# Kernel optimization log

Hardware: AMD Instinct MI355X
Metric: run time of the kernel (lower is better)

Reference implementation:

```python
import jax, jax.numpy as jnp
import numpy as np

B, N, C = 16, 4096, 1024
K = 64
TEMPERATURE = 1.0


def setup_inputs() -> dict:
    key = jax.random.key(0)
    kx, kw = jax.random.split(key)
    x = jax.random.normal(kx, (B, N, C), dtype=jnp.float32)
    # nn.Linear(dim, dim): W is (out, in), b is (out,)
    W = jax.random.normal(kw, (C, C), dtype=jnp.float32) * (1.0 / np.sqrt(C))
    b = jnp.zeros((C,), dtype=jnp.float32)
    return {"x": x, "W": W, "b": b}


def reference(x, W, b):
    Bv, Nv, Cv = x.shape
    # proj = x @ W.T + b ; scores = proj.mean(-1)  -> fold mean into a single matvec:
    # mean(x W^T + b) = x @ (mean of W rows) + mean(b), but keep faithful/explicit form.
    proj = jnp.einsum('bnc,dc->bnd', x, W) + b          # (B, N, C)
    scores = jnp.mean(proj, axis=-1)                    # (B, N)
    k = min(K, Nv)
    _, topk_idx = jax.lax.top_k(scores, k)              # (B, k)
    mask = jnp.zeros_like(scores).at[jnp.arange(Bv)[:, None], topk_idx].set(1.0)
    attn = jax.nn.softmax(scores / TEMPERATURE, axis=-1) * mask  # (B, N)
    out = jnp.einsum('bn,bnc->bc', attn, x)             # (B, C)
    return out, mask
```

## Files before the change

kernel.cpp:

```cpp
#include <hip/hip_runtime.h>
#include <cstdint>

#define B_ 16
#define N_ 4096
#define C_ 1024
#define K_ 64

typedef float vf4 __attribute__((ext_vector_type(4)));

#define WS_WBAR   0
#define WS_BBAR   1024
#define WS_SCORES 2048
#define WS_TIDX   (WS_SCORES + B_*N_)
#define WS_TATT   (WS_TIDX + B_*K_)
#define WS_PART   (WS_TATT + B_*K_)

__global__ __launch_bounds__(256) void wsum1_kernel(const float* __restrict__ W,
                                                    const float* __restrict__ b,
                                                    float* __restrict__ ws) {
    int j = blockIdx.x, t = threadIdx.x;
    if (j == 64) {
        float4 bv = ((const float4*)b)[t];
        float sb = bv.x + bv.y + bv.z + bv.w;
        for (int off = 32; off; off >>= 1) sb += __shfl_xor(sb, off);
        __shared__ float red[4];
        if ((t & 63) == 0) red[t >> 6] = sb;
        __syncthreads();
        if (t == 0) ws[WS_BBAR] = (red[0] + red[1] + red[2] + red[3]) * (1.0f / C_);
        return;
    }
    const float4* W4 = (const float4*)W;
    float4 s = {0.f, 0.f, 0.f, 0.f};
#pragma unroll
    for (int d = 0; d < 16; ++d) {
        float4 w = W4[(j * 16 + d) * 256 + t];
        s.x += w.x; s.y += w.y; s.z += w.z; s.w += w.w;
    }
    ((float4*)(ws + WS_PART))[j * 256 + t] = s;
}

__global__ __launch_bounds__(256) void wsum2_kernel(float* __restrict__ ws) {
    int col = blockIdx.x * 256 + threadIdx.x;
    float s = 0.f;
#pragma unroll 8
    for (int j = 0; j < 64; ++j) s += ws[WS_PART + j * 1024 + col];
    ws[WS_WBAR + col] = s * (1.0f / C_);
}

__global__ __launch_bounds__(512) void scores_kernel(const float* __restrict__ x,
                                                     float* ws) {
    __shared__ float lw[C_];
    int t = threadIdx.x;
    float bbar = ws[WS_BBAR];
    if (t < 256) ((float4*)lw)[t] = ((const float4*)(ws + WS_WBAR))[t];
    __syncthreads();
    int wave = t >> 6, lane = t & 63;
    int row = blockIdx.x * 8 + wave;
    const vf4* x4 = (const vf4*)x;
    const float4* lw4 = (const float4*)lw;
    float acc = 0.f;
#pragma unroll
    for (int q = 0; q < 4; ++q) {
        vf4 xv = __builtin_nontemporal_load(x4 + (size_t)row * 256 + q * 64 + lane);
        float4 wv = lw4[q * 64 + lane];
        acc += xv.x * wv.x + xv.y * wv.y + xv.z * wv.z + xv.w * wv.w;
    }
    for (int off = 32; off; off >>= 1) acc += __shfl_xor(acc, off);
    if (lane == 0) ws[WS_SCORES + row] = acc + bbar;
}

__device__ __forceinline__ unsigned su_(float f) {
    unsigned u = __float_as_uint(f);
    return (u & 0x80000000u) ? ~u : (u | 0x80000000u);
}
__device__ __forceinline__ float isu_(unsigned u) {
    unsigned v = (u & 0x80000000u) ? (u ^ 0x80000000u) : ~u;
    return __uint_as_float(v);
}

__global__ __launch_bounds__(256) void topk_kernel(float* ws,
                                                   float* __restrict__ mask_out) {
    __shared__ unsigned hist[4096];
    __shared__ unsigned long long cand[4096];
    __shared__ float redf[4];
    __shared__ unsigned scnt;
    __shared__ int sbin;
    int b = blockIdx.x, t = threadIdx.x;
    int wid = t >> 6, lane = t & 63;
    const float* srow = ws + WS_SCORES + b * N_;

    float v[16];
#pragma unroll
    for (int e = 0; e < 16; ++e) v[e] = srow[e * 256 + t];

#pragma unroll
    for (int e = 0; e < 16; ++e) hist[e * 256 + t] = 0;
    if (t == 0) scnt = 0;

    float m = v[0];
#pragma unroll
    for (int e = 1; e < 16; ++e) m = fmaxf(m, v[e]);
    for (int off = 32; off; off >>= 1) m = fmaxf(m, __shfl_xor(m, off));
    if (lane == 0) redf[wid] = m;
    __syncthreads();
    m = fmaxf(fmaxf(redf[0], redf[1]), fmaxf(redf[2], redf[3]));

    float dsum = 0.f;
#pragma unroll
    for (int e = 0; e < 16; ++e) dsum += expf(v[e] - m);
    for (int off = 32; off; off >>= 1) dsum += __shfl_xor(dsum, off);

#pragma unroll
    for (int e = 0; e < 16; ++e) atomicAdd(&hist[su_(v[e]) >> 20], 1u);

    __syncthreads();
    if (lane == 0) redf[wid] = dsum;
    __syncthreads();
    float denom = redf[0] + redf[1] + redf[2] + redf[3];

    if (wid == 0) {
        int base = lane * 64;
        unsigned s = 0;
        for (int j = 0; j < 64; ++j) s += hist[base + j];
        unsigned suf = s;
        for (int off = 1; off < 64; off <<= 1) {
            unsigned o = __shfl_down(suf, off);
            if (lane + off < 64) suf += o;
        }
        unsigned above = suf - s;
        if (above < (unsigned)K_ && above + s >= (unsigned)K_) {
            unsigned run = above;
            for (int j = 63; j >= 0; --j) {
                unsigned c = hist[base + j];
                if (run < (unsigned)K_ && run + c >= (unsigned)K_) sbin = base + j;
                run += c;
            }
        }
    }
    __syncthreads();
    int Bn = sbin;

#pragma unroll
    for (int e = 0; e < 16; ++e) {
        unsigned k32 = su_(v[e]);
        if ((int)(k32 >> 20) >= Bn) {
            unsigned p = atomicAdd(&scnt, 1u);
            cand[p] = ((unsigned long long)k32 << 32) |
                      (unsigned long long)(0xFFFFFFFFu - (unsigned)(e * 256 + t));
        }
    }
#pragma unroll
    for (int e = 0; e < 16; ++e) mask_out[b * N_ + e * 256 + t] = 0.0f;
    __syncthreads();

    unsigned mc = scnt;
    int*   tidx = (int*)ws + WS_TIDX;
    float* tatt = ws + WS_TATT;
    for (unsigned i = t; i < mc; i += 256) {
        unsigned long long ki = cand[i];
        unsigned r = 0;
        for (unsigned j = 0; j < mc; ++j) r += (cand[j] > ki) ? 1u : 0u;
        if (r < (unsigned)K_) {
            unsigned widx = 0xFFFFFFFFu - (unsigned)(ki & 0xFFFFFFFFu);
            float sc = isu_((unsigned)(ki >> 32));
            tidx[b * K_ + r] = (int)widx;
            tatt[b * K_ + r] = expf(sc - m) / denom;
            mask_out[b * N_ + widx] = 1.0f;
        }
    }
}

__global__ __launch_bounds__(256) void out_kernel(const float* __restrict__ x,
                                                  const float* __restrict__ ws,
                                                  float* __restrict__ out) {
    int blk = blockIdx.x;
    int b = blk >> 2, cc = blk & 3;
    int t = threadIdx.x;
    __shared__ int   li[K_];
    __shared__ float la[K_];
    if (t < K_) {
        li[t] = ((const int*)ws + WS_TIDX)[b * K_ + t];
        la[t] = (ws + WS_TATT)[b * K_ + t];
    }
    __syncthreads();
    int col = cc * 256 + t;
    float acc = 0.f;
#pragma unroll 8
    for (int r = 0; r < K_; ++r) {
        acc += la[r] * x[(size_t)(b * N_ + li[r]) * C_ + col];
    }
    out[b * C_ + col] = acc;
}

extern "C" void kernel_launch(void* const* d_in, const int* in_sizes, int n_in,
                              void* d_out, int out_size, void* d_ws, size_t ws_size,
                              hipStream_t stream) {
    const float* x = (const float*)d_in[0];
    const float* W = (const float*)d_in[1];
    const float* b = (const float*)d_in[2];
    float* out  = (float*)d_out;
    float* mask = out + B_ * C_;
    float* ws   = (float*)d_ws;

    wsum1_kernel <<<65,           256, 0, stream>>>(W, b, ws);
    wsum2_kernel <<<4,            256, 0, stream>>>(ws);
    scores_kernel<<<B_ * N_ / 8,  512, 0, stream>>>(x, ws);
    topk_kernel  <<<B_,           256, 0, stream>>>(ws, mask);
    out_kernel   <<<B_ * 4,       256, 0, stream>>>(x, ws, out);
}
```

Before: 65.24 us.

## Fuse top-k and output gather, compute row max in scores kernel

Merges the top-k selection and the weighted gather of x rows into one 1024-thread kernel per batch, so the selected indices and weights stay in shared memory instead of going through the workspace, and one launch is dropped. Each scores block now also atomically folds its maximum into a per-batch max, which removes the max reduction pass from the top-k kernel. Wider blocks mean each thread handles 4 scores instead of 16. The output gather now runs in only 16 blocks, which may limit bandwidth for that phase.

```diff
diff --git a/kernel.cpp b/kernel.cpp
--- a/kernel.cpp
+++ b/kernel.cpp
@@ -11,15 +11,24 @@
 #define WS_WBAR   0
 #define WS_BBAR   1024
 #define WS_SCORES 2048
-#define WS_TIDX   (WS_SCORES + B_*N_)
-#define WS_TATT   (WS_TIDX + B_*K_)
-#define WS_PART   (WS_TATT + B_*K_)
+#define WS_BMAX   (WS_SCORES + B_*N_)
+#define WS_PART   (WS_BMAX + B_)
+
+__device__ __forceinline__ unsigned su_(float f) {
+    unsigned u = __float_as_uint(f);
+    return (u & 0x80000000u) ? ~u : (u | 0x80000000u);
+}
+__device__ __forceinline__ float isu_(unsigned u) {
+    unsigned v = (u & 0x80000000u) ? (u ^ 0x80000000u) : ~u;
+    return __uint_as_float(v);
+}
 
 __global__ __launch_bounds__(256) void wsum1_kernel(const float* __restrict__ W,
                                                     const float* __restrict__ b,
                                                     float* __restrict__ ws) {
     int j = blockIdx.x, t = threadIdx.x;
     if (j == 64) {
+        if (t < B_) ((unsigned*)(ws + WS_BMAX))[t] = 0u;
         float4 bv = ((const float4*)b)[t];
         float sb = bv.x + bv.y + bv.z + bv.w;
         for (int off = 32; off; off >>= 1) sb += __shfl_xor(sb, off);
@@ -50,6 +59,7 @@
 __global__ __launch_bounds__(512) void scores_kernel(const float* __restrict__ x,
                                                      float* ws) {
     __shared__ float lw[C_];
+    __shared__ float smax[8];
     int t = threadIdx.x;
     float bbar = ws[WS_BBAR];
     if (t < 256) ((float4*)lw)[t] = ((const float4*)(ws + WS_WBAR))[t];
@@ -66,57 +76,62 @@
         acc += xv.x * wv.x + xv.y * wv.y + xv.z * wv.z + xv.w * wv.w;
     }
     for (int off = 32; off; off >>= 1) acc += __shfl_xor(acc, off);
-    if (lane == 0) ws[WS_SCORES + row] = acc + bbar;
-}
-
-__device__ __forceinline__ unsigned su_(float f) {
-    unsigned u = __float_as_uint(f);
-    return (u & 0x80000000u) ? ~u : (u | 0x80000000u);
-}
-__device__ __forceinline__ float isu_(unsigned u) {
-    unsigned v = (u & 0x80000000u) ? (u ^ 0x80000000u) : ~u;
-    return __uint_as_float(v);
-}
-
-__global__ __launch_bounds__(256) void topk_kernel(float* ws,
-                                                   float* __restrict__ mask_out) {
+    float sc = acc + bbar;
+    if (lane == 0) {
+        ws[WS_SCORES + row] = sc;
+        smax[wave] = sc;
+    }
+    __syncthreads();
+    if (t == 0) {
+        float m = smax[0];
+#pragma unroll
+        for (int i = 1; i < 8; ++i) m = fmaxf(m, smax[i]);
+        atomicMax((unsigned*)(ws + WS_BMAX) + (blockIdx.x >> 9), su_(m));
+    }
+}
+
+__global__ __launch_bounds__(1024) void topk_out_kernel(const float* __restrict__ x,
+                                                        float* ws,
+                                                        float* __restrict__ out,
+                                                        float* __restrict__ mask_out) {
     __shared__ unsigned hist[4096];
     __shared__ unsigned long long cand[4096];
-    __shared__ float redf[4];
+    __shared__ float redf[16];
+    __shared__ float sdenom;
     __shared__ unsigned scnt;
     __shared__ int sbin;
+    __shared__ int   li[K_];
+    __shared__ float la[K_];
     int b = blockIdx.x, t = threadIdx.x;
     int wid = t >> 6, lane = t & 63;
     const float* srow = ws + WS_SCORES + b * N_;
 
-    float v[16];
-#pragma unroll
-    for (int e = 0; e < 16; ++e) v[e] = srow[e * 256 + t];
-
-#pragma unroll
-    for (int e = 0; e < 16; ++e) hist[e * 256 + t] = 0;
+    float m = isu_(((const unsigned*)(ws + WS_BMAX))[b]);
+
+    float4 v4 = ((const float4*)srow)[t];
+    float v[4] = {v4.x, v4.y, v4.z, v4.w};
+
+    ((uint4*)hist)[t] = make_uint4(0u, 0u, 0u, 0u);
     if (t == 0) scnt = 0;
 
-    float m = v[0];
-#pragma unroll
-    for (int e = 1; e < 16; ++e) m = fmaxf(m, v[e]);
-    for (int off = 32; off; off >>= 1) m = fmaxf(m, __shfl_xor(m, off));
-    if (lane == 0) redf[wid] = m;
-    __syncthreads();
-    m = fmaxf(fmaxf(redf[0], redf[1]), fmaxf(redf[2], redf[3]));
-
     float dsum = 0.f;
 #pragma unroll
-    for (int e = 0; e < 16; ++e) dsum += expf(v[e] - m);
+    for (int e = 0; e < 4; ++e) dsum += expf(v[e] - m);
     for (int off = 32; off; off >>= 1) dsum += __shfl_xor(dsum, off);
-
-#pragma unroll
-    for (int e = 0; e < 16; ++e) atomicAdd(&hist[su_(v[e]) >> 20], 1u);
-
-    __syncthreads();
     if (lane == 0) redf[wid] = dsum;
-    __syncthreads();
-    float denom = redf[0] + redf[1] + redf[2] + redf[3];
+
+    __syncthreads();
+    if (t == 0) {
+        float s = redf[0];
+#pragma unroll
+        for (int i = 1; i < 16; ++i) s += redf[i];
+        sdenom = s;
+    }
+
+#pragma unroll
+    for (int e = 0; e < 4; ++e) atomicAdd(&hist[su_(v[e]) >> 20], 1u);
+    __syncthreads();
+    float denom = sdenom;
 
     if (wid == 0) {
         int base = lane * 64;
@@ -141,55 +156,38 @@
     int Bn = sbin;
 
 #pragma unroll
-    for (int e = 0; e < 16; ++e) {
+    for (int e = 0; e < 4; ++e) {
         unsigned k32 = su_(v[e]);
         if ((int)(k32 >> 20) >= Bn) {
             unsigned p = atomicAdd(&scnt, 1u);
             cand[p] = ((unsigned long long)k32 << 32) |
-                      (unsigned long long)(0xFFFFFFFFu - (unsigned)(e * 256 + t));
-        }
-    }
-#pragma unroll
-    for (int e = 0; e < 16; ++e) mask_out[b * N_ + e * 256 + t] = 0.0f;
+                      (unsigned long long)(0xFFFFFFFFu - (unsigned)(4 * t + e));
+        }
+    }
+    ((float4*)(mask_out + b * N_))[t] = make_float4(0.f, 0.f, 0.f, 0.f);
     __syncthreads();
 
     unsigned mc = scnt;
-    int*   tidx = (int*)ws + WS_TIDX;
-    float* tatt = ws + WS_TATT;
-    for (unsigned i = t; i < mc; i += 256) {
+    for (unsigned i = t; i < mc; i += 1024) {
         unsigned long long ki = cand[i];
         unsigned r = 0;
         for (unsigned j = 0; j < mc; ++j) r += (cand[j] > ki) ? 1u : 0u;
         if (r < (unsigned)K_) {
             unsigned widx = 0xFFFFFFFFu - (unsigned)(ki & 0xFFFFFFFFu);
             float sc = isu_((unsigned)(ki >> 32));
-            tidx[b * K_ + r] = (int)widx;
-            tatt[b * K_ + r] = expf(sc - m) / denom;
+            li[r] = (int)widx;
+            la[r] = expf(sc - m) / denom;
             mask_out[b * N_ + widx] = 1.0f;
         }
     }
-}
-
-__global__ __launch_bounds__(256) void out_kernel(const float* __restrict__ x,
-                                                  const float* __restrict__ ws,
-                                                  float* __restrict__ out) {
-    int blk = blockIdx.x;
-    int b = blk >> 2, cc = blk & 3;
-    int t = threadIdx.x;
-    __shared__ int   li[K_];
-    __shared__ float la[K_];
-    if (t < K_) {
-        li[t] = ((const int*)ws + WS_TIDX)[b * K_ + t];
-        la[t] = (ws + WS_TATT)[b * K_ + t];
-    }
-    __syncthreads();
-    int col = cc * 256 + t;
+    __syncthreads();
+
     float acc = 0.f;
 #pragma unroll 8
     for (int r = 0; r < K_; ++r) {
-        acc += la[r] * x[(size_t)(b * N_ + li[r]) * C_ + col];
-    }
-    out[b * C_ + col] = acc;
+        acc += la[r] * x[(size_t)(b * N_ + li[r]) * C_ + t];
+    }
+    out[b * C_ + t] = acc;
 }
 
 extern "C" void kernel_launch(void* const* d_in, const int* in_sizes, int n_in,
@@ -202,9 +200,8 @@
     float* mask = out + B_ * C_;
     float* ws   = (float*)d_ws;
 
-    wsum1_kernel <<<65,           256, 0, stream>>>(W, b, ws);
-    wsum2_kernel <<<4,            256, 0, stream>>>(ws);
-    scores_kernel<<<B_ * N_ / 8,  512, 0, stream>>>(x, ws);
-    topk_kernel  <<<B_,           256, 0, stream>>>(ws, mask);
-    out_kernel   <<<B_ * 4,       256, 0, stream>>>(x, ws, out);
-}
+    wsum1_kernel   <<<65,          256, 0, stream>>>(W, b, ws);
+    wsum2_kernel   <<<4,           256, 0, stream>>>(ws);
+    scores_kernel  <<<B_ * N_ / 8, 512, 0, stream>>>(x, ws);
+    topk_out_kernel<<<B_,          1024, 0, stream>>>(x, ws, out, mask);
+}
```

After: 128.6 us. 1.97x slower.
